# Performance work log

Measured on AMD Instinct MI355X. Metric: run time of the kernel, lower is better.

## Reference

```python
import jax, jax.numpy as jnp
import numpy as np

B, C, H, W = 32, 64, 128, 128

def setup_inputs() -> dict:
    key = jax.random.key(0)
    k1, k2, k3, k4 = jax.random.split(key, 4)
    x = jax.random.normal(k1, (B, C, H, W), dtype=jnp.float32)
    theta = jax.random.normal(k2, (C, C), dtype=jnp.float32) * (6.0 / (C + C)) ** 0.5  # xavier-ish
    W_lin = jax.random.normal(k3, (C, C), dtype=jnp.float32) * (1.0 / C) ** 0.5
    b_lin = jax.random.normal(k4, (C,), dtype=jnp.float32) * 0.01
    return {"x": x, "theta": theta, "W_lin": W_lin, "b_lin": b_lin}

def reference(x, theta, W_lin, b_lin):
    b, c, h, w = x.shape
    # channel descriptor: global average pool -> [B, C]
    wvec = jnp.mean(x, axis=(2, 3))
    # pairwise diff and soft adjacency, batched over B
    diff = wvec[:, :, None] - wvec[:, None, :]              # [B, C, C]
    e = jnp.exp(-diff)
    T = jnp.abs(1.0 - e / (1.0 + e)) - 1.0                  # [B, C, C]
    A = 0.5 * (T + jnp.swapaxes(T, 1, 2)) * theta           # [B, C, C]
    # graph conv: A @ x_flat, relu
    x_flat = x.reshape(b, c, h * w)                         # [B, C, HW]
    Hmat = jax.nn.relu(jnp.einsum('bij,bjn->bin', A, x_flat))  # [B, C, HW]
    # Linear over channel dim applied to H.T: [B, HW, C]
    Hout = jnp.einsum('bin,ci->bnc', Hmat, W_lin) + b_lin   # [B, HW, C]
    # faithful to torch: H.view(C, h, w) is a raw row-major reshape of [HW, C]
    return Hout.reshape(b, c, h, w)
```

## Files before the change

kernel.cpp:

```cpp
#include <hip/hip_runtime.h>

static constexpr int Cc  = 64;
static constexpr int HWc = 16384;
static constexpr int Bc  = 32;
static constexpr int NT  = 128;
static constexpr int TPB = 4;


typedef _Float16 v8h __attribute__((ext_vector_type(8)));
typedef float    v4f __attribute__((ext_vector_type(4)));

union FragU { uint32_t u[4]; v8h h; };

__device__ inline uint32_t packf2(float lo, float hi) {
  union { _Float16 h[2]; uint32_t u; } r;
  r.h[0] = (_Float16)lo; r.h[1] = (_Float16)hi;
  return r.u;
}

__device__ inline v4f mfma16(v8h a, v8h b, v4f c) {
  return __builtin_amdgcn_mfma_f32_16x16x32_f16(a, b, c, 0, 0, 0);
}

__global__ void prep_weights(const float* __restrict__ theta,
                             const float* __restrict__ Wlin,
                             _Float16* __restrict__ M1h,
                             _Float16* __restrict__ Wh) {
  int t = blockIdx.x * 256 + threadIdx.x;
  if (t < Cc * Cc) {
    M1h[t] = (_Float16)(-0.5f * theta[t]);
    Wh[t]  = (_Float16)(Wlin[t]);
  }
}

__global__ __launch_bounds__(256, 3) void fused_mfma(
    const float* __restrict__ x,
    const _Float16* __restrict__ M1h,
    const _Float16* __restrict__ Wh,
    const float* __restrict__ blin,
    float* __restrict__ out)
{
  __shared__ __align__(16) uint32_t  xp[2][32][132];
  __shared__ __align__(16) _Float16  p2[4][32][72];

  const int tid   = threadIdx.x;
  const int tile0 = blockIdx.x * TPB;
  const int b     = tile0 >> 7;
  const int n00   = (tile0 & 127) * NT;
  const float* xb = x + (size_t)b * Cc * HWc;

  const int wv   = tid >> 6;
  const int lq   = tid & 15;
  const int quad = (tid & 63) >> 4;
  const int nw   = wv * 32;

  const int sp   = tid >> 5;
  const int scol = (tid & 31) * 4;

  {
    const float* xt = xb + n00;
#pragma unroll
    for (int rep = 0; rep < 4; ++rep) {
      const int p = rep * 8 + sp;
      const float4 e = *(const float4*)(xt + (size_t)(2 * p)     * HWc + scol);
      const float4 o = *(const float4*)(xt + (size_t)(2 * p + 1) * HWc + scol);
      uint4 w;
      w.x = packf2(e.x, o.x); w.y = packf2(e.y, o.y);
      w.z = packf2(e.z, o.z); w.w = packf2(e.w, o.w);
      *(uint4*)&xp[0][p][scol] = w;
    }
  }

  const v8h* M1v = (const v8h*)M1h;
  const v8h* Whv = (const v8h*)Wh;
  v8h w1[4][2], w2[4][2];
#pragma unroll
  for (int it = 0; it < 4; ++it)
#pragma unroll
    for (int kt = 0; kt < 2; ++kt) {
      w1[it][kt] = M1v[(it * 16 + lq) * 8 + kt * 4 + quad];
      w2[it][kt] = Whv[(it * 16 + lq) * 8 + kt * 4 + quad];
    }
  v4f bias4[4];
#pragma unroll
  for (int ct = 0; ct < 4; ++ct)
    bias4[ct] = *(const v4f*)(blin + ct * 16 + quad * 4);

  __syncthreads();

#pragma unroll
  for (int t = 0; t < TPB; ++t) {
    const int cur = t & 1;

    float4 pf[8];
    if (t < TPB - 1) {
      const float* xt = xb + n00 + (t + 1) * NT;
#pragma unroll
      for (int rep = 0; rep < 4; ++rep) {
        const int p = rep * 8 + sp;
        pf[2 * rep]     = *(const float4*)(xt + (size_t)(2 * p)     * HWc + scol);
        pf[2 * rep + 1] = *(const float4*)(xt + (size_t)(2 * p + 1) * HWc + scol);
      }
    }

    FragU xf[2][2];
#pragma unroll
    for (int nt = 0; nt < 2; ++nt)
#pragma unroll
      for (int kt = 0; kt < 2; ++kt)
#pragma unroll
        for (int r = 0; r < 4; ++r)
          xf[nt][kt].u[r] = xp[cur][kt * 16 + quad * 4 + r][nw + nt * 16 + lq];

#pragma unroll
    for (int it = 0; it < 4; ++it)
#pragma unroll
      for (int nt = 0; nt < 2; ++nt) {
        v4f a = {0.f, 0.f, 0.f, 0.f};
#pragma unroll
        for (int kt = 0; kt < 2; ++kt)
          a = mfma16(w1[it][kt], xf[nt][kt].h, a);
        uint2 w;
        w.x = packf2(fmaxf(a[0], 0.f), fmaxf(a[1], 0.f));
        w.y = packf2(fmaxf(a[2], 0.f), fmaxf(a[3], 0.f));
        *(uint2*)&p2[wv][nt * 16 + lq][it * 16 + quad * 4] = w;
      }

    const size_t orow0 = ((size_t)b * HWc + n00 + t * NT + nw) * Cc;
#pragma unroll
    for (int nt = 0; nt < 2; ++nt) {
      FragU pr[2];
#pragma unroll
      for (int kt = 0; kt < 2; ++kt)
        pr[kt].h = *(const v8h*)&p2[wv][nt * 16 + lq][kt * 32 + quad * 8];
      float* orow = out + orow0 + (size_t)(nt * 16 + lq) * Cc + quad * 4;
#pragma unroll
      for (int ct = 0; ct < 4; ++ct) {
        v4f a = bias4[ct];
#pragma unroll
        for (int kt = 0; kt < 2; ++kt)
          a = mfma16(w2[ct][kt], pr[kt].h, a);
        *(v4f*)(orow + ct * 16) = a;
      }
    }

    if (t < TPB - 1) {
#pragma unroll
      for (int rep = 0; rep < 4; ++rep) {
        const int p = rep * 8 + sp;
        uint4 w;
        w.x = packf2(pf[2 * rep].x, pf[2 * rep + 1].x);
        w.y = packf2(pf[2 * rep].y, pf[2 * rep + 1].y);
        w.z = packf2(pf[2 * rep].z, pf[2 * rep + 1].z);
        w.w = packf2(pf[2 * rep].w, pf[2 * rep + 1].w);
        *(uint4*)&xp[cur ^ 1][p][scol] = w;
      }
      __syncthreads();
    }
  }
}

extern "C" void kernel_launch(void* const* d_in, const int* in_sizes, int n_in,
                              void* d_out, int out_size, void* d_ws, size_t ws_size,
                              hipStream_t stream) {
  const float* x     = (const float*)d_in[0];
  const float* theta = (const float*)d_in[1];
  const float* W_lin = (const float*)d_in[2];
  const float* b_lin = (const float*)d_in[3];
  float* out = (float*)d_out;

  _Float16* M1h = (_Float16*)d_ws;
  _Float16* Wh  = M1h + Cc * Cc;

  prep_weights<<<(Cc * Cc + 255) / 256, 256, 0, stream>>>(theta, W_lin, M1h, Wh);

  const int nblocks = Bc * HWc / (NT * TPB);
  fused_mfma<<<nblocks, 256, 0, stream>>>(x, M1h, Wh, b_lin, out);
}
```

Baseline: 246.4 us.

## Give each wave a private pixel strip, drop block barriers, stage W_lin in LDS

After: 249.0 us. About the same (+1.1%).

```diff
diff --git a/kernel.cpp b/kernel.cpp
--- a/kernel.cpp
+++ b/kernel.cpp
@@ -3,8 +3,6 @@
 static constexpr int Cc  = 64;
 static constexpr int HWc = 16384;
 static constexpr int Bc  = 32;
-static constexpr int NT  = 128;
-static constexpr int TPB = 4;
 
 
 typedef _Float16 v8h __attribute__((ext_vector_type(8)));
@@ -33,129 +31,127 @@
   }
 }
 
-__global__ __launch_bounds__(256, 3) void fused_mfma(
+__global__ __launch_bounds__(256, 4) void fused_mfma(
     const float* __restrict__ x,
     const _Float16* __restrict__ M1h,
     const _Float16* __restrict__ Wh,
     const float* __restrict__ blin,
     float* __restrict__ out)
 {
-  __shared__ __align__(16) uint32_t  xp[2][32][132];
-  __shared__ __align__(16) _Float16  p2[4][32][72];
+  __shared__ __align__(16) uint32_t xp[4][32][36];
+  __shared__ __align__(16) _Float16 p2[4][16][72];
+  __shared__ __align__(16) _Float16 w2l[64][72];
 
-  const int tid   = threadIdx.x;
-  const int tile0 = blockIdx.x * TPB;
-  const int b     = tile0 >> 7;
-  const int n00   = (tile0 & 127) * NT;
-  const float* xb = x + (size_t)b * Cc * HWc;
+  const int tid  = threadIdx.x;
+  const int wv   = tid >> 6;
+  const int l    = tid & 63;
+  const int lq   = tid & 15;
+  const int quad = l >> 4;
 
-  const int wv   = tid >> 6;
-  const int lq   = tid & 15;
-  const int quad = (tid & 63) >> 4;
-  const int nw   = wv * 32;
-
-  const int sp   = tid >> 5;
-  const int scol = (tid & 31) * 4;
+  const int b     = blockIdx.x >> 5;
+  const int npix0 = (blockIdx.x & 31) * 512 + wv * 128;
+  const float* xb = x + (size_t)b * Cc * HWc + npix0;
 
   {
-    const float* xt = xb + n00;
-#pragma unroll
-    for (int rep = 0; rep < 4; ++rep) {
-      const int p = rep * 8 + sp;
-      const float4 e = *(const float4*)(xt + (size_t)(2 * p)     * HWc + scol);
-      const float4 o = *(const float4*)(xt + (size_t)(2 * p + 1) * HWc + scol);
-      uint4 w;
-      w.x = packf2(e.x, o.x); w.y = packf2(e.y, o.y);
-      w.z = packf2(e.z, o.z); w.w = packf2(e.w, o.w);
-      *(uint4*)&xp[0][p][scol] = w;
-    }
+    const int r = tid >> 2, seg = (tid & 3) * 16;
+    const uint4* wg = (const uint4*)(Wh + r * 64 + seg);
+    uint4 a0 = wg[0], a1 = wg[1];
+    *(uint4*)&w2l[r][seg]     = a0;
+    *(uint4*)&w2l[r][seg + 8] = a1;
   }
 
   const v8h* M1v = (const v8h*)M1h;
-  const v8h* Whv = (const v8h*)Wh;
-  v8h w1[4][2], w2[4][2];
+  v8h w1[4][2];
 #pragma unroll
   for (int it = 0; it < 4; ++it)
 #pragma unroll
-    for (int kt = 0; kt < 2; ++kt) {
+    for (int kt = 0; kt < 2; ++kt)
       w1[it][kt] = M1v[(it * 16 + lq) * 8 + kt * 4 + quad];
-      w2[it][kt] = Whv[(it * 16 + lq) * 8 + kt * 4 + quad];
-    }
   v4f bias4[4];
 #pragma unroll
   for (int ct = 0; ct < 4; ++ct)
     bias4[ct] = *(const v4f*)(blin + ct * 16 + quad * 4);
 
+  const int sp_ = l >> 3;
+  const int sc  = (l & 7) * 4;
+
+#pragma unroll
+  for (int rep = 0; rep < 4; ++rep) {
+    const int p = rep * 8 + sp_;
+    const float4 e = *(const float4*)(xb + (size_t)(2 * p)     * HWc + sc);
+    const float4 o = *(const float4*)(xb + (size_t)(2 * p + 1) * HWc + sc);
+    uint4 w;
+    w.x = packf2(e.x, o.x); w.y = packf2(e.y, o.y);
+    w.z = packf2(e.z, o.z); w.w = packf2(e.w, o.w);
+    *(uint4*)&xp[wv][p][sc] = w;
+  }
+
   __syncthreads();
 
 #pragma unroll
-  for (int t = 0; t < TPB; ++t) {
-    const int cur = t & 1;
-
+  for (int t = 0; t < 4; ++t) {
     float4 pf[8];
-    if (t < TPB - 1) {
-      const float* xt = xb + n00 + (t + 1) * NT;
+    if (t < 3) {
+      const float* xt = xb + (t + 1) * 32;
 #pragma unroll
       for (int rep = 0; rep < 4; ++rep) {
-        const int p = rep * 8 + sp;
-        pf[2 * rep]     = *(const float4*)(xt + (size_t)(2 * p)     * HWc + scol);
-        pf[2 * rep + 1] = *(const float4*)(xt + (size_t)(2 * p + 1) * HWc + scol);
+        const int p = rep * 8 + sp_;
+        pf[2 * rep]     = *(const float4*)(xt + (size_t)(2 * p)     * HWc + sc);
+        pf[2 * rep + 1] = *(const float4*)(xt + (size_t)(2 * p + 1) * HWc + sc);
       }
     }
 
-    FragU xf[2][2];
 #pragma unroll
-    for (int nt = 0; nt < 2; ++nt)
+    for (int nt = 0; nt < 2; ++nt) {
+      FragU xf[2];
 #pragma unroll
       for (int kt = 0; kt < 2; ++kt)
 #pragma unroll
         for (int r = 0; r < 4; ++r)
-          xf[nt][kt].u[r] = xp[cur][kt * 16 + quad * 4 + r][nw + nt * 16 + lq];
+          xf[kt].u[r] = xp[wv][kt * 16 + quad * 4 + r][nt * 16 + lq];
 
 #pragma unroll
-    for (int it = 0; it < 4; ++it)
-#pragma unroll
-      for (int nt = 0; nt < 2; ++nt) {
+      for (int it = 0; it < 4; ++it) {
         v4f a = {0.f, 0.f, 0.f, 0.f};
 #pragma unroll
         for (int kt = 0; kt < 2; ++kt)
-          a = mfma16(w1[it][kt], xf[nt][kt].h, a);
+          a = mfma16(w1[it][kt], xf[kt].h, a);
         uint2 w;
         w.x = packf2(fmaxf(a[0], 0.f), fmaxf(a[1], 0.f));
         w.y = packf2(fmaxf(a[2], 0.f), fmaxf(a[3], 0.f));
-        *(uint2*)&p2[wv][nt * 16 + lq][it * 16 + quad * 4] = w;
+        *(uint2*)&p2[wv][lq][it * 16 + quad * 4] = w;
       }
 
-    const size_t orow0 = ((size_t)b * HWc + n00 + t * NT + nw) * Cc;
-#pragma unroll
-    for (int nt = 0; nt < 2; ++nt) {
       FragU pr[2];
 #pragma unroll
       for (int kt = 0; kt < 2; ++kt)
-        pr[kt].h = *(const v8h*)&p2[wv][nt * 16 + lq][kt * 32 + quad * 8];
-      float* orow = out + orow0 + (size_t)(nt * 16 + lq) * Cc + quad * 4;
+        pr[kt].h = *(const v8h*)&p2[wv][lq][kt * 32 + quad * 8];
+
+      float* orow = out + ((size_t)b * HWc + npix0 + t * 32 + nt * 16 + lq) * Cc
+                    + quad * 4;
 #pragma unroll
       for (int ct = 0; ct < 4; ++ct) {
         v4f a = bias4[ct];
 #pragma unroll
-        for (int kt = 0; kt < 2; ++kt)
-          a = mfma16(w2[ct][kt], pr[kt].h, a);
+        for (int kt = 0; kt < 2; ++kt) {
+          const v8h b2 = *(const v8h*)&w2l[ct * 16 + lq][kt * 32 + quad * 8];
+          a = mfma16(b2, pr[kt].h, a);
+        }
         *(v4f*)(orow + ct * 16) = a;
       }
     }
 
-    if (t < TPB - 1) {
+    if (t < 3) {
 #pragma unroll
       for (int rep = 0; rep < 4; ++rep) {
-        const int p = rep * 8 + sp;
+        const int p = rep * 8 + sp_;
         uint4 w;
         w.x = packf2(pf[2 * rep].x, pf[2 * rep + 1].x);
         w.y = packf2(pf[2 * rep].y, pf[2 * rep + 1].y);
         w.z = packf2(pf[2 * rep].z, pf[2 * rep + 1].z);
         w.w = packf2(pf[2 * rep].w, pf[2 * rep + 1].w);
-        *(uint4*)&xp[cur ^ 1][p][scol] = w;
+        *(uint4*)&xp[wv][p][sc] = w;
       }
-      __syncthreads();
     }
   }
 }
@@ -174,6 +170,6 @@
 
   prep_weights<<<(Cc * Cc + 255) / 256, 256, 0, stream>>>(theta, W_lin, M1h, Wh);
 
-  const int nblocks = Bc * HWc / (NT * TPB);
+  const int nblocks = Bc * HWc / 512;
   fused_mfma<<<nblocks, 256, 0, stream>>>(x, M1h, Wh, b_lin, out);
 }
```
